# Kernel optimization log

Hardware: AMD Instinct MI355X
Metric: run time of the kernel (lower is better)

## Reference

```python
import jax, jax.numpy as jnp
import numpy as np

# Dims (match init_kwargs / input_specs)
B, S, HID = 1, 2048, 2048
NH, NKV, HD = 16, 4, 128          # head_dim = HID // NH
REP = NH // NKV                    # num_key_value_groups
BLOCK_SIZE, LOCAL_BLOCKS, SINK_NUM = 8, 4, 4
SCALING = HD ** -0.5


def rotate_half(x):
    x1, x2 = jnp.split(x, 2, axis=-1)
    return jnp.concatenate([-x2, x1], axis=-1)


def setup_inputs() -> dict:
    key = jax.random.key(0)
    ks = jax.random.split(key, 7)
    return {
        "hidden_states": jax.random.normal(ks[0], (B, S, HID), jnp.float32),
        "cos": jax.random.uniform(ks[1], (B, S, HD), jnp.float32, minval=-1.0, maxval=1.0),
        "sin": jax.random.uniform(ks[2], (B, S, HD), jnp.float32, minval=-1.0, maxval=1.0),
        # Projection weights stored as [in, out] so x @ W matches nn.Linear (bias=False).
        "Wq": 0.02 * jax.random.normal(ks[3], (HID, NH * HD), jnp.float32),
        "Wk": 0.02 * jax.random.normal(ks[4], (HID, NKV * HD), jnp.float32),
        "Wv": 0.02 * jax.random.normal(ks[5], (HID, NKV * HD), jnp.float32),
        "Wo": 0.02 * jax.random.normal(ks[6], (NH * HD, HID), jnp.float32),
    }


def sink_local_mask(seq_len):
    # query i attends to: sink tokens j < min(SINK_NUM, i), and local window
    # max(0, i - LOCAL_BLOCKS*BLOCK_SIZE) <= j <= i (diagonal included so every
    # row has at least one valid key; see notes).
    i = jnp.arange(seq_len)[:, None]
    j = jnp.arange(seq_len)[None, :]
    sink = j < jnp.minimum(SINK_NUM, i)
    local = (j >= i - LOCAL_BLOCKS * BLOCK_SIZE) & (j <= i)
    return sink | local  # [S, S] bool, broadcast over (B, H)


def reference(hidden_states, cos, sin, Wq, Wk, Wv, Wo):
    # projections -> [B, H, S, D]
    q = (hidden_states @ Wq).reshape(B, S, NH, HD).transpose(0, 2, 1, 3)
    k = (hidden_states @ Wk).reshape(B, S, NKV, HD).transpose(0, 2, 1, 3)
    v = (hidden_states @ Wv).reshape(B, S, NKV, HD).transpose(0, 2, 1, 3)
    # rotary embedding, cos/sin broadcast over head dim (unsqueeze_dim=1)
    c = cos[:, None, :, :]
    s = sin[:, None, :, :]
    q = q * c + rotate_half(q) * s
    k = k * c + rotate_half(k) * s
    # repeat_kv (GQA) -> [B, NH, S, D]
    k = jnp.repeat(k, REP, axis=1)
    v = jnp.repeat(v, REP, axis=1)
    # sink + local sparse attention (dense compute + mask, as in source)
    scores = jnp.einsum('bhqd,bhkd->bhqk', q, k) * SCALING
    mask = sink_local_mask(S)
    scores = jnp.where(mask, scores, -jnp.inf)
    attn_weights = jax.nn.softmax(scores, axis=-1)
    attn_output = jnp.einsum('bhqk,bhkd->bhqd', attn_weights, v)
    # Faithful to source: view(B, S, -1) on the [B, H, S, D] layout WITHOUT a
    # transpose(1,2) first (the original code omits it).
    attn_output = attn_output.reshape(B, S, NH * HD)
    attn_output = attn_output @ Wo
    return attn_output, attn_weights
```

## Files before the change

kernel.cpp:

```cpp
#include <hip/hip_runtime.h>

typedef unsigned short ushort_t;
typedef __attribute__((ext_vector_type(8))) short short8;
typedef __attribute__((ext_vector_type(4))) float f32x4;
typedef __attribute__((ext_vector_type(8))) unsigned short us8;
typedef __attribute__((ext_vector_type(4))) unsigned short us4;

#define SEQ 2048
#define HIDD 2048
#define XLD 3072
#define SCALING 0.08838834764831843f
#define KSPLIT 1024

__device__ __forceinline__ float bf2f(ushort_t u) {
    unsigned int x = ((unsigned int)u) << 16;
    return __builtin_bit_cast(float, x);
}
__device__ __forceinline__ ushort_t f2bf(float f) {
    unsigned int u = __builtin_bit_cast(unsigned int, f);
    u += 0x7fffu + ((u >> 16) & 1u);
    return (ushort_t)(u >> 16);
}

__global__ __launch_bounds__(256) void cvt_f32_bf16(
    const float* __restrict__ in, ushort_t* __restrict__ out, int n) {
    int i = (blockIdx.x * 256 + threadIdx.x) * 4;
    if (i < n) {
        float4 v = *(const float4*)(in + i);
        us4 o;
        o[0] = f2bf(v.x); o[1] = f2bf(v.y); o[2] = f2bf(v.z); o[3] = f2bf(v.w);
        *(us4*)(out + i) = o;
    }
}

__device__ __forceinline__ void transpose_tile(
    const float* __restrict__ W, ushort_t* __restrict__ Wt,
    int N, int n0, int k0, int dstRow0) {
    __shared__ ushort_t t[64 * 80];
    const int tid = threadIdx.x;
    {
        const int kl = tid >> 4;
        const int nc = (tid & 15) * 4;
        #pragma unroll
        for (int p = 0; p < 4; ++p) {
            int k = kl + p * 16;
            float4 v = *(const float4*)(W + (size_t)(k0 + k) * N + n0 + nc);
            t[(nc + 0) * 80 + k] = f2bf(v.x);
            t[(nc + 1) * 80 + k] = f2bf(v.y);
            t[(nc + 2) * 80 + k] = f2bf(v.z);
            t[(nc + 3) * 80 + k] = f2bf(v.w);
        }
    }
    __syncthreads();
    {
        const int nl = tid >> 3;
        const int kc = (tid & 7) * 8;
        #pragma unroll
        for (int p = 0; p < 2; ++p) {
            int n = nl + p * 32;
            *(us8*)(Wt + (size_t)(dstRow0 + n) * HIDD + k0 + kc) =
                *(const us8*)&t[n * 80 + kc];
        }
    }
}

__global__ __launch_bounds__(256) void transpose_qkv(
    const float* __restrict__ Wq, const float* __restrict__ Wk,
    const float* __restrict__ Wv, ushort_t* __restrict__ Wt) {
    int bx = blockIdx.x, k0 = blockIdx.y * 64;
    if (bx < 32)       transpose_tile(Wq, Wt, 2048, bx * 64,        k0, bx * 64);
    else if (bx < 40)  transpose_tile(Wk, Wt, 512,  (bx - 32) * 64, k0, 2048 + (bx - 32) * 64);
    else               transpose_tile(Wv, Wt, 512,  (bx - 40) * 64, k0, 2560 + (bx - 40) * 64);
}

__global__ __launch_bounds__(256) void transpose_wo(
    const float* __restrict__ Wo, ushort_t* __restrict__ Wt) {
    transpose_tile(Wo, Wt, 2048, blockIdx.x * 64, blockIdx.y * 64, blockIdx.x * 64);
}

__global__ __launch_bounds__(256) void gemm_splitk(
    const ushort_t* __restrict__ A, int lda,
    const ushort_t* __restrict__ Bt, int ldb,
    float* __restrict__ P, int ldc) {
    __shared__ ushort_t lA[128 * 32];
    __shared__ ushort_t lB[128 * 32];
    const int tid = threadIdx.x;
    const int wave = tid >> 6, lane = tid & 63;
    const int wm = wave >> 1, wn = wave & 1;
    const int quad = lane >> 4, l16 = lane & 15;
    const int m0 = blockIdx.y * 128, n0 = blockIdx.x * 128;
    const int z = blockIdx.z;

    A  += (size_t)z * KSPLIT;
    Bt += (size_t)z * KSPLIT;
    P  += (size_t)z * ((size_t)gridDim.y * 128) * ldc;

    const int srow = lane >> 2;
    const int scol = 8 * ((lane & 3) ^ (srow & 3));

    f32x4 acc[4][4] = {};

    const ushort_t* Ab = A  + (size_t)(m0 + wave * 16 + srow) * lda + scol;
    const ushort_t* Bb = Bt + (size_t)(n0 + wave * 16 + srow) * ldb + scol;
    ushort_t* lAw = lA + (wave * 16) * 32;
    ushort_t* lBw = lB + (wave * 16) * 32;

    const int rsw = (quad ^ (l16 & 3)) * 8;

    for (int kk = 0; kk < KSPLIT; kk += 32) {
        __syncthreads();
        #pragma unroll
        for (int c = 0; c < 2; ++c) {
            __builtin_amdgcn_global_load_lds(
                (const __attribute__((address_space(1))) unsigned int*)(const void*)
                    (Ab + (size_t)(c * 64) * lda + kk),
                (__attribute__((address_space(3))) unsigned int*)(void*)
                    (lAw + c * 64 * 32), 16, 0, 0);
            __builtin_amdgcn_global_load_lds(
                (const __attribute__((address_space(1))) unsigned int*)(const void*)
                    (Bb + (size_t)(c * 64) * ldb + kk),
                (__attribute__((address_space(3))) unsigned int*)(void*)
                    (lBw + c * 64 * 32), 16, 0, 0);
        }
        __syncthreads();
        short8 af[4], bfr[4];
        #pragma unroll
        for (int mt = 0; mt < 4; ++mt)
            af[mt] = *(const short8*)&lA[(wm * 64 + mt * 16 + l16) * 32 + rsw];
        #pragma unroll
        for (int nt = 0; nt < 4; ++nt)
            bfr[nt] = *(const short8*)&lB[(wn * 64 + nt * 16 + l16) * 32 + rsw];
        #pragma unroll
        for (int mt = 0; mt < 4; ++mt) {
            #pragma unroll
            for (int nt = 0; nt < 4; ++nt)
                acc[mt][nt] = __builtin_amdgcn_mfma_f32_16x16x32_bf16(
                    af[mt], bfr[nt], acc[mt][nt], 0, 0, 0);
        }
    }

    #pragma unroll
    for (int mt = 0; mt < 4; ++mt) {
        #pragma unroll
        for (int nt = 0; nt < 4; ++nt) {
            int gm = m0 + wm * 64 + mt * 16 + quad * 4;
            int gn = n0 + wn * 64 + nt * 16 + l16;
            #pragma unroll
            for (int r = 0; r < 4; ++r)
                P[(size_t)(gm + r) * ldc + gn] = acc[mt][nt][r];
        }
    }
}

__global__ __launch_bounds__(256) void reduce_rope_qk(
    const float* __restrict__ P, ushort_t* __restrict__ X,
    const float* __restrict__ cosp, const float* __restrict__ sinp) {
    const size_t ZS = (size_t)SEQ * XLD;
    int idx = blockIdx.x * 256 + threadIdx.x;
    int d = idx & 63;
    int rem = idx >> 6;
    int hh = rem % 20;
    int s = rem / 20;
    int cb = (hh < 16) ? hh * 128 : 2048 + (hh - 16) * 128;
    size_t base = (size_t)s * XLD + cb;
    float x1 = P[base + d] + P[ZS + base + d];
    float x2 = P[base + d + 64] + P[ZS + base + d + 64];
    const float* cr = cosp + (size_t)s * 128;
    const float* sr = sinp + (size_t)s * 128;
    X[base + d]      = f2bf(x1 * cr[d]      - x2 * sr[d]);
    X[base + d + 64] = f2bf(x2 * cr[d + 64] + x1 * sr[d + 64]);
}

__global__ __launch_bounds__(256) void reduce_v(
    const float* __restrict__ P, ushort_t* __restrict__ X) {
    const size_t ZS = (size_t)SEQ * XLD;
    int idx = (blockIdx.x * 256 + threadIdx.x) * 4;
    int c = idx & 511;
    int s = idx >> 9;
    size_t base = (size_t)s * XLD + 2560 + c;
    float4 a = *(const float4*)(P + base);
    float4 b = *(const float4*)(P + ZS + base);
    us4 o;
    o[0] = f2bf(a.x + b.x); o[1] = f2bf(a.y + b.y);
    o[2] = f2bf(a.z + b.z); o[3] = f2bf(a.w + b.w);
    *(us4*)(X + base) = o;
}

__global__ __launch_bounds__(256) void reduce_out(
    const float* __restrict__ P, float* __restrict__ out) {
    const size_t ZS = (size_t)SEQ * HIDD;
    int idx = (blockIdx.x * 256 + threadIdx.x) * 4;
    float4 a = *(const float4*)(P + idx);
    float4 b = *(const float4*)(P + ZS + idx);
    float4 o; o.x = a.x + b.x; o.y = a.y + b.y; o.z = a.z + b.z; o.w = a.w + b.w;
    *(float4*)(out + idx) = o;
}

__global__ __launch_bounds__(256) void attn_kernel(
    const ushort_t* __restrict__ X, float* __restrict__ Wts,
    ushort_t* __restrict__ Aout) {
    int g = blockIdx.x * 4 + (threadIdx.x >> 6);
    int lane = threadIdx.x & 63;
    int i = g & (SEQ - 1);
    int h = g >> 11;

    const ushort_t* Q = X + (size_t)i * XLD + h * 128;
    unsigned int qv = *(const unsigned int*)(Q + 2 * lane);
    float q0 = bf2f((ushort_t)(qv & 0xffff));
    float q1 = bf2f((ushort_t)(qv >> 16));

    int lo = i - 32; if (lo < 0) lo = 0;
    int nsink = lo < 4 ? lo : 4;
    int NJ = nsink + (i - lo + 1);

    const ushort_t* Kbase = X + 2048 + (h >> 2) * 128;
    const ushort_t* Vbase = X + 2560 + (h >> 2) * 128;

    float m = -1e30f, mysc = -1e30f;
    for (int jj = 0; jj < NJ; ++jj) {
        int j = (jj < nsink) ? jj : (lo + jj - nsink);
        unsigned int kv = *(const unsigned int*)(Kbase + (size_t)j * XLD + 2 * lane);
        float p = q0 * bf2f((ushort_t)(kv & 0xffff)) + q1 * bf2f((ushort_t)(kv >> 16));
        #pragma unroll
        for (int off = 32; off > 0; off >>= 1) p += __shfl_xor(p, off, 64);
        p *= SCALING;
        if (jj == lane) mysc = p;
        m = fmaxf(m, p);
    }
    float e = (lane < NJ) ? expf(mysc - m) : 0.f;
    float l = e;
    #pragma unroll
    for (int off = 32; off > 0; off >>= 1) l += __shfl_xor(l, off, 64);
    float w = e / l;

    float* row = Wts + ((size_t)h * SEQ + i) * SEQ;
    #pragma unroll
    for (int s = 0; s < 8; ++s) {
        float4 o;
        #pragma unroll
        for (int t = 0; t < 4; ++t) {
            int c = s * 256 + lane * 4 + t;
            bool in = (c < nsink) || (c >= lo && c <= i);
            int jjc = in ? ((c < nsink) ? c : (nsink + c - lo)) : 0;
            float wv = __shfl(w, jjc, 64);
            o[t] = in ? wv : 0.f;
        }
        *(float4*)(row + s * 256 + lane * 4) = o;
    }

    float o0 = 0.f, o1 = 0.f;
    for (int jj = 0; jj < NJ; ++jj) {
        int j = (jj < nsink) ? jj : (lo + jj - nsink);
        float pb = __shfl(w, jj, 64);
        unsigned int vv = *(const unsigned int*)(Vbase + (size_t)j * XLD + 2 * lane);
        o0 += pb * bf2f((ushort_t)(vv & 0xffff));
        o1 += pb * bf2f((ushort_t)(vv >> 16));
    }
    int r = h * 128 + (i >> 4);
    int c = (i & 15) * 128 + 2 * lane;
    ushort_t* Ar = Aout + (size_t)r * HIDD + c;
    Ar[0] = f2bf(o0);
    Ar[1] = f2bf(o1);
}

extern "C" void kernel_launch(void* const* d_in, const int* in_sizes, int n_in,
                              void* d_out, int out_size, void* d_ws, size_t ws_size,
                              hipStream_t stream) {
    if (n_in < 7) return;
    const float* hid  = (const float*)d_in[0];
    const float* cosp = (const float*)d_in[1];
    const float* sinp = (const float*)d_in[2];
    const float* Wq   = (const float*)d_in[3];
    const float* Wk   = (const float*)d_in[4];
    const float* Wv   = (const float*)d_in[5];
    const float* Wo   = (const float*)d_in[6];

    float* out = (float*)d_out;
    float* wts = out + (size_t)SEQ * HIDD;

    ushort_t* Hb    = (ushort_t*)d_ws;
    ushort_t* Wqkvt = Hb    + (size_t)2048 * 2048;
    ushort_t* Wot   = Wqkvt + (size_t)3072 * 2048;
    ushort_t* X     = Wot   + (size_t)2048 * 2048;
    ushort_t* Am    = X     + (size_t)SEQ * XLD;
    float*    Pqkv  = (float*)(Am + (size_t)SEQ * HIDD);
    float*    Pout  = Pqkv + 2 * (size_t)SEQ * XLD;
    size_t need = ((char*)(Pout + 2 * (size_t)SEQ * HIDD)) - (char*)d_ws;
    if (ws_size < need) return;

    dim3 blk(256);
    cvt_f32_bf16<<<(HIDD * SEQ) / (256 * 4), blk, 0, stream>>>(hid, Hb, HIDD * SEQ);
    transpose_qkv<<<dim3(48, 32), blk, 0, stream>>>(Wq, Wk, Wv, Wqkvt);
    transpose_wo<<<dim3(32, 32), blk, 0, stream>>>(Wo, Wot);

    gemm_splitk<<<dim3(24, 16, 2), blk, 0, stream>>>(Hb, HIDD, Wqkvt, 2048, Pqkv, XLD);
    reduce_rope_qk<<<(SEQ * 20 * 64) / 256, blk, 0, stream>>>(Pqkv, X, cosp, sinp);
    reduce_v<<<(SEQ * 512) / (256 * 4), blk, 0, stream>>>(Pqkv, X);

    attn_kernel<<<(SEQ * 16) / 4, blk, 0, stream>>>(X, wts, Am);

    gemm_splitk<<<dim3(16, 16, 2), blk, 0, stream>>>(Am, HIDD, Wot, 2048, Pout, HIDD);
    reduce_out<<<(SEQ * HIDD) / (256 * 4), blk, 0, stream>>>(Pout, out);
}
```

Baseline: 547.3 us.

## Merge transpose/reduce kernels, double K-step per barrier, 3-way split-K output GEMM

Combines the QKV and Wo weight transposes into one launch and the RoPE and V reductions into one launch. The GEMM now loads two 32-wide K slices per barrier pair, halving synchronisation, and takes per-split K extents so the output projection can use an uneven 3-way split-K. That split adds more blocks for occupancy, at the cost of an extra partial buffer to reduce and double the LDS per block.

```diff
diff --git a/kernel.cpp b/kernel.cpp
--- a/kernel.cpp
+++ b/kernel.cpp
@@ -10,7 +10,6 @@
 #define HIDD 2048
 #define XLD 3072
 #define SCALING 0.08838834764831843f
-#define KSPLIT 1024
 
 __device__ __forceinline__ float bf2f(ushort_t u) {
     unsigned int x = ((unsigned int)u) << 16;
@@ -64,26 +63,24 @@
     }
 }
 
-__global__ __launch_bounds__(256) void transpose_qkv(
+__global__ __launch_bounds__(256) void transpose_all(
     const float* __restrict__ Wq, const float* __restrict__ Wk,
-    const float* __restrict__ Wv, ushort_t* __restrict__ Wt) {
+    const float* __restrict__ Wv, const float* __restrict__ Wo,
+    ushort_t* __restrict__ Wqkvt, ushort_t* __restrict__ Wot) {
     int bx = blockIdx.x, k0 = blockIdx.y * 64;
-    if (bx < 32)       transpose_tile(Wq, Wt, 2048, bx * 64,        k0, bx * 64);
-    else if (bx < 40)  transpose_tile(Wk, Wt, 512,  (bx - 32) * 64, k0, 2048 + (bx - 32) * 64);
-    else               transpose_tile(Wv, Wt, 512,  (bx - 40) * 64, k0, 2560 + (bx - 40) * 64);
-}
-
-__global__ __launch_bounds__(256) void transpose_wo(
-    const float* __restrict__ Wo, ushort_t* __restrict__ Wt) {
-    transpose_tile(Wo, Wt, 2048, blockIdx.x * 64, blockIdx.y * 64, blockIdx.x * 64);
+    if (bx < 32)       transpose_tile(Wq, Wqkvt, 2048, bx * 64,        k0, bx * 64);
+    else if (bx < 40)  transpose_tile(Wk, Wqkvt, 512,  (bx - 32) * 64, k0, 2048 + (bx - 32) * 64);
+    else if (bx < 48)  transpose_tile(Wv, Wqkvt, 512,  (bx - 40) * 64, k0, 2560 + (bx - 40) * 64);
+    else               transpose_tile(Wo, Wot,   2048, (bx - 48) * 64, k0, (bx - 48) * 64);
 }
 
 __global__ __launch_bounds__(256) void gemm_splitk(
     const ushort_t* __restrict__ A, int lda,
     const ushort_t* __restrict__ Bt, int ldb,
-    float* __restrict__ P, int ldc) {
-    __shared__ ushort_t lA[128 * 32];
-    __shared__ ushort_t lB[128 * 32];
+    float* __restrict__ P, int ldc,
+    int koff_unit, const int4 kexts) {
+    __shared__ ushort_t lA[2 * 128 * 32];
+    __shared__ ushort_t lB[2 * 128 * 32];
     const int tid = threadIdx.x;
     const int wave = tid >> 6, lane = tid & 63;
     const int wm = wave >> 1, wn = wave & 1;
@@ -91,8 +88,14 @@
     const int m0 = blockIdx.y * 128, n0 = blockIdx.x * 128;
     const int z = blockIdx.z;
 
-    A  += (size_t)z * KSPLIT;
-    Bt += (size_t)z * KSPLIT;
+    const int ke[4] = {kexts.x, kexts.y, kexts.z, kexts.w};
+    int koff = 0;
+    for (int zz = 0; zz < 4; ++zz) if (zz < z) koff += ke[zz];
+    const int kext = ke[z];
+    (void)koff_unit;
+
+    A  += (size_t)koff;
+    Bt += (size_t)koff;
     P  += (size_t)z * ((size_t)gridDim.y * 128) * ldc;
 
     const int srow = lane >> 2;
@@ -107,35 +110,41 @@
 
     const int rsw = (quad ^ (l16 & 3)) * 8;
 
-    for (int kk = 0; kk < KSPLIT; kk += 32) {
+    for (int kk = 0; kk < kext; kk += 64) {
         __syncthreads();
         #pragma unroll
-        for (int c = 0; c < 2; ++c) {
-            __builtin_amdgcn_global_load_lds(
-                (const __attribute__((address_space(1))) unsigned int*)(const void*)
-                    (Ab + (size_t)(c * 64) * lda + kk),
-                (__attribute__((address_space(3))) unsigned int*)(void*)
-                    (lAw + c * 64 * 32), 16, 0, 0);
-            __builtin_amdgcn_global_load_lds(
-                (const __attribute__((address_space(1))) unsigned int*)(const void*)
-                    (Bb + (size_t)(c * 64) * ldb + kk),
-                (__attribute__((address_space(3))) unsigned int*)(void*)
-                    (lBw + c * 64 * 32), 16, 0, 0);
+        for (int kh = 0; kh < 2; ++kh) {
+            #pragma unroll
+            for (int c = 0; c < 2; ++c) {
+                __builtin_amdgcn_global_load_lds(
+                    (const __attribute__((address_space(1))) unsigned int*)(const void*)
+                        (Ab + (size_t)(c * 64) * lda + kk + kh * 32),
+                    (__attribute__((address_space(3))) unsigned int*)(void*)
+                        (lAw + kh * 128 * 32 + c * 64 * 32), 16, 0, 0);
+                __builtin_amdgcn_global_load_lds(
+                    (const __attribute__((address_space(1))) unsigned int*)(const void*)
+                        (Bb + (size_t)(c * 64) * ldb + kk + kh * 32),
+                    (__attribute__((address_space(3))) unsigned int*)(void*)
+                        (lBw + kh * 128 * 32 + c * 64 * 32), 16, 0, 0);
+            }
         }
         __syncthreads();
-        short8 af[4], bfr[4];
-        #pragma unroll
-        for (int mt = 0; mt < 4; ++mt)
-            af[mt] = *(const short8*)&lA[(wm * 64 + mt * 16 + l16) * 32 + rsw];
-        #pragma unroll
-        for (int nt = 0; nt < 4; ++nt)
-            bfr[nt] = *(const short8*)&lB[(wn * 64 + nt * 16 + l16) * 32 + rsw];
-        #pragma unroll
-        for (int mt = 0; mt < 4; ++mt) {
+        #pragma unroll
+        for (int kh = 0; kh < 2; ++kh) {
+            short8 af[4], bfr[4];
+            #pragma unroll
+            for (int mt = 0; mt < 4; ++mt)
+                af[mt] = *(const short8*)&lA[kh * 128 * 32 + (wm * 64 + mt * 16 + l16) * 32 + rsw];
             #pragma unroll
             for (int nt = 0; nt < 4; ++nt)
-                acc[mt][nt] = __builtin_amdgcn_mfma_f32_16x16x32_bf16(
-                    af[mt], bfr[nt], acc[mt][nt], 0, 0, 0);
+                bfr[nt] = *(const short8*)&lB[kh * 128 * 32 + (wn * 64 + nt * 16 + l16) * 32 + rsw];
+            #pragma unroll
+            for (int mt = 0; mt < 4; ++mt) {
+                #pragma unroll
+                for (int nt = 0; nt < 4; ++nt)
+                    acc[mt][nt] = __builtin_amdgcn_mfma_f32_16x16x32_bf16(
+                        af[mt], bfr[nt], acc[mt][nt], 0, 0, 0);
+            }
         }
     }
 
@@ -152,47 +161,49 @@
     }
 }
 
-__global__ __launch_bounds__(256) void reduce_rope_qk(
+#define ROPE_THREADS (SEQ * 20 * 64)
+__global__ __launch_bounds__(256) void reduce_x(
     const float* __restrict__ P, ushort_t* __restrict__ X,
     const float* __restrict__ cosp, const float* __restrict__ sinp) {
     const size_t ZS = (size_t)SEQ * XLD;
     int idx = blockIdx.x * 256 + threadIdx.x;
-    int d = idx & 63;
-    int rem = idx >> 6;
-    int hh = rem % 20;
-    int s = rem / 20;
-    int cb = (hh < 16) ? hh * 128 : 2048 + (hh - 16) * 128;
-    size_t base = (size_t)s * XLD + cb;
-    float x1 = P[base + d] + P[ZS + base + d];
-    float x2 = P[base + d + 64] + P[ZS + base + d + 64];
-    const float* cr = cosp + (size_t)s * 128;
-    const float* sr = sinp + (size_t)s * 128;
-    X[base + d]      = f2bf(x1 * cr[d]      - x2 * sr[d]);
-    X[base + d + 64] = f2bf(x2 * cr[d + 64] + x1 * sr[d + 64]);
-}
-
-__global__ __launch_bounds__(256) void reduce_v(
-    const float* __restrict__ P, ushort_t* __restrict__ X) {
-    const size_t ZS = (size_t)SEQ * XLD;
-    int idx = (blockIdx.x * 256 + threadIdx.x) * 4;
-    int c = idx & 511;
-    int s = idx >> 9;
-    size_t base = (size_t)s * XLD + 2560 + c;
-    float4 a = *(const float4*)(P + base);
-    float4 b = *(const float4*)(P + ZS + base);
-    us4 o;
-    o[0] = f2bf(a.x + b.x); o[1] = f2bf(a.y + b.y);
-    o[2] = f2bf(a.z + b.z); o[3] = f2bf(a.w + b.w);
-    *(us4*)(X + base) = o;
-}
-
-__global__ __launch_bounds__(256) void reduce_out(
+    if (idx < ROPE_THREADS) {
+        int d = idx & 63;
+        int rem = idx >> 6;
+        int hh = rem % 20;
+        int s = rem / 20;
+        int cb = (hh < 16) ? hh * 128 : 2048 + (hh - 16) * 128;
+        size_t base = (size_t)s * XLD + cb;
+        float x1 = P[base + d] + P[ZS + base + d];
+        float x2 = P[base + d + 64] + P[ZS + base + d + 64];
+        const float* cr = cosp + (size_t)s * 128;
+        const float* sr = sinp + (size_t)s * 128;
+        X[base + d]      = f2bf(x1 * cr[d]      - x2 * sr[d]);
+        X[base + d + 64] = f2bf(x2 * cr[d + 64] + x1 * sr[d + 64]);
+    } else {
+        int v = (idx - ROPE_THREADS) * 4;
+        int c = v & 511;
+        int s = v >> 9;
+        size_t base = (size_t)s * XLD + 2560 + c;
+        float4 a = *(const float4*)(P + base);
+        float4 b = *(const float4*)(P + ZS + base);
+        us4 o;
+        o[0] = f2bf(a.x + b.x); o[1] = f2bf(a.y + b.y);
+        o[2] = f2bf(a.z + b.z); o[3] = f2bf(a.w + b.w);
+        *(us4*)(X + base) = o;
+    }
+}
+
+__global__ __launch_bounds__(256) void reduce_out3(
     const float* __restrict__ P, float* __restrict__ out) {
     const size_t ZS = (size_t)SEQ * HIDD;
     int idx = (blockIdx.x * 256 + threadIdx.x) * 4;
     float4 a = *(const float4*)(P + idx);
     float4 b = *(const float4*)(P + ZS + idx);
-    float4 o; o.x = a.x + b.x; o.y = a.y + b.y; o.z = a.z + b.z; o.w = a.w + b.w;
+    float4 c = *(const float4*)(P + 2 * ZS + idx);
+    float4 o;
+    o.x = a.x + b.x + c.x; o.y = a.y + b.y + c.y;
+    o.z = a.z + b.z + c.z; o.w = a.w + b.w + c.w;
     *(float4*)(out + idx) = o;
 }
 
@@ -285,20 +296,21 @@
     ushort_t* Am    = X     + (size_t)SEQ * XLD;
     float*    Pqkv  = (float*)(Am + (size_t)SEQ * HIDD);
     float*    Pout  = Pqkv + 2 * (size_t)SEQ * XLD;
-    size_t need = ((char*)(Pout + 2 * (size_t)SEQ * HIDD)) - (char*)d_ws;
+    size_t need = ((char*)(Pout + 3 * (size_t)SEQ * HIDD)) - (char*)d_ws;
     if (ws_size < need) return;
 
     dim3 blk(256);
     cvt_f32_bf16<<<(HIDD * SEQ) / (256 * 4), blk, 0, stream>>>(hid, Hb, HIDD * SEQ);
-    transpose_qkv<<<dim3(48, 32), blk, 0, stream>>>(Wq, Wk, Wv, Wqkvt);
-    transpose_wo<<<dim3(32, 32), blk, 0, stream>>>(Wo, Wot);
-
-    gemm_splitk<<<dim3(24, 16, 2), blk, 0, stream>>>(Hb, HIDD, Wqkvt, 2048, Pqkv, XLD);
-    reduce_rope_qk<<<(SEQ * 20 * 64) / 256, blk, 0, stream>>>(Pqkv, X, cosp, sinp);
-    reduce_v<<<(SEQ * 512) / (256 * 4), blk, 0, stream>>>(Pqkv, X);
+    transpose_all<<<dim3(80, 32), blk, 0, stream>>>(Wq, Wk, Wv, Wo, Wqkvt, Wot);
+
+    gemm_splitk<<<dim3(24, 16, 2), blk, 0, stream>>>(
+        Hb, HIDD, Wqkvt, 2048, Pqkv, XLD, 0, make_int4(1024, 1024, 0, 0));
+    reduce_x<<<(ROPE_THREADS + SEQ * 512 / 4 + 255) / 256, blk, 0, stream>>>(
+        Pqkv, X, cosp, sinp);
 
     attn_kernel<<<(SEQ * 16) / 4, blk, 0, stream>>>(X, wts, Am);
 
-    gemm_splitk<<<dim3(16, 16, 2), blk, 0, stream>>>(Am, HIDD, Wot, 2048, Pout, HIDD);
-    reduce_out<<<(SEQ * HIDD) / (256 * 4), blk, 0, stream>>>(Pout, out);
-}
+    gemm_splitk<<<dim3(16, 16, 3), blk, 0, stream>>>(
+        Am, HIDD, Wot, 2048, Pout, HIDD, 0, make_int4(704, 704, 640, 0));
+    reduce_out3<<<(SEQ * HIDD) / (256 * 4), blk, 0, stream>>>(Pout, out);
+}
```

New measurement: 531.0 us. -3.0%, faster.
